# Performance work log

Hardware: AMD Instinct MI355X
Metric: run time of the kernel (lower is better)

The kernel has to match this reference:

```python
import jax, jax.numpy as jnp
import numpy as np

B, IN, H = 16384, 512, 512


def setup_inputs() -> dict:
    key = jax.random.key(0)
    ks = jax.random.split(key, 7)
    s_in = 1.0 / np.sqrt(IN)
    s_h = 1.0 / np.sqrt(H)
    return {
        "x": jax.random.normal(ks[0], (B, IN), jnp.float32),
        "h": jax.random.normal(ks[1], (B, H), jnp.float32),
        "c": jax.random.normal(ks[2], (B, H), jnp.float32),
        # packed gate weights, order [i, f, g, o] along last dim (4*H)
        "Wx": jax.random.normal(ks[3], (IN, 4 * H), jnp.float32) * s_in,
        "Wh": jax.random.normal(ks[4], (H, 4 * H), jnp.float32) * s_h,
        "bx": jax.random.normal(ks[5], (4 * H,), jnp.float32) * s_in,
        "bh": jax.random.normal(ks[6], (4 * H,), jnp.float32) * s_h,
    }


def reference(x, h, c, Wx, Wh, bx, bh):
    # one fused GEMM per input stream instead of 8 small linears; same math
    gates = x @ Wx + bx + h @ Wh + bh          # [B, 4H]
    gi, gf, gg, go = jnp.split(gates, 4, axis=-1)
    i = jax.nn.sigmoid(gi)
    f = jax.nn.sigmoid(gf)
    g = jnp.tanh(gg)
    o = jax.nn.sigmoid(go)
    c_new = f * c + i * g
    h_new = o * jnp.tanh(c_new)
    return (h_new, c_new)
```

## Files before the change

### kernel.cpp

```cpp
#include <hip/hip_runtime.h>
#include <hip/hip_bf16.h>

#define B_DIM   16384
#define IN_DIM  512
#define H_DIM   512
#define K_DIM   1024
#define N4H     2048
#define BH      (B_DIM * H_DIM)

typedef __attribute__((ext_vector_type(8))) short  short8;
typedef __attribute__((ext_vector_type(4))) short  short4v;
typedef __attribute__((ext_vector_type(4))) float  f32x4;

__device__ inline void async_load16(const void* g, void* l) {
    __builtin_amdgcn_global_load_lds(
        (const __attribute__((address_space(1))) void*)g,
        (__attribute__((address_space(3)))       void*)l, 16, 0, 0);
}

__device__ inline short bf16bits(float f) {
    __hip_bfloat16 b = __float2bfloat16(f);
    return *reinterpret_cast<short*>(&b);
}

__device__ inline float sigmoidf_(float v) {
    return 1.0f / (1.0f + __expf(-v));
}
__device__ inline float tanhf_(float v) {
    v = fminf(fmaxf(v, -30.f), 30.f);
    float e = __expf(2.f * v);
    return (e - 1.f) / (e + 1.f);
}

__global__ __launch_bounds__(256) void prep_all(
    const float* __restrict__ Wx, const float* __restrict__ Wh,
    const float* __restrict__ bx, const float* __restrict__ bh,
    const float* __restrict__ x,  const float* __restrict__ h,
    __hip_bfloat16* __restrict__ Wt, __hip_bfloat16* __restrict__ Axh,
    float* __restrict__ bias_p) {
    const int bid = blockIdx.x;
    const int t   = threadIdx.x;

    if (bid < 2048) {
        __shared__ __hip_bfloat16 tile[32][33];
        const int bk = bid & 31;
        const int bn = bid >> 5;
        const int kb = bk * 32, nb = bn * 32;
#pragma unroll
        for (int r = 0; r < 4; ++r) {
            int k_loc = r * 8 + (t >> 5);
            int n_loc = t & 31;
            int kg = kb + k_loc;
            float v = (kg < IN_DIM) ? Wx[(size_t)kg * N4H + nb + n_loc]
                                    : Wh[(size_t)(kg - IN_DIM) * N4H + nb + n_loc];
            tile[k_loc][n_loc] = __float2bfloat16(v);
        }
        __syncthreads();
        {
            int n_loc = t >> 3;
            int k_loc = (t & 7) * 4;
            int ng = nb + n_loc;
            int g  = ng >> 9;
            int c  = ng & 511;
            int row_out = (c >> 5) * 128 + g * 32 + (c & 31);
            short4v v4;
            v4.x = *reinterpret_cast<short*>(&tile[k_loc + 0][n_loc]);
            v4.y = *reinterpret_cast<short*>(&tile[k_loc + 1][n_loc]);
            v4.z = *reinterpret_cast<short*>(&tile[k_loc + 2][n_loc]);
            v4.w = *reinterpret_cast<short*>(&tile[k_loc + 3][n_loc]);
            *(short4v*)&Wt[(size_t)row_out * K_DIM + kb + k_loc] = v4;
        }
        if (bid < 8) {
            int ng = bid * 256 + t;
            int g  = ng >> 9;
            int c  = ng & 511;
            int ro = (c >> 5) * 128 + g * 32 + (c & 31);
            bias_p[ro] = bx[ng] + bh[ng];
        }
    } else {
        const int ab = bid - 2048;
        const int kq = t;
        const float* src = (kq < 128) ? (x + kq * 4)
                                      : (h + (size_t)(kq - 128) * 4);
#pragma unroll
        for (int j = 0; j < 8; ++j) {
            int m = ab * 8 + j;
            float4 v = *(const float4*)(src + (size_t)m * 512);
            short4v sv;
            sv.x = bf16bits(v.x);
            sv.y = bf16bits(v.y);
            sv.z = bf16bits(v.z);
            sv.w = bf16bits(v.w);
            *(short4v*)&Axh[(size_t)m * K_DIM + kq * 4] = sv;
        }
    }
}

__global__ __launch_bounds__(512, 2) void lstm_gemm256(
    const float* __restrict__ c_in,
    const __hip_bfloat16* __restrict__ Axh,
    const __hip_bfloat16* __restrict__ Wt,
    const float* __restrict__ bias_p,
    float* __restrict__ out) {
    __shared__ __align__(16) __hip_bfloat16 lds_a[2][16384];
    __shared__ __align__(16) __hip_bfloat16 lds_b[2][16384];

    const int tid   = threadIdx.x;
    const int w     = tid >> 6;
    const int lane  = tid & 63;
    const int col16 = lane & 15;
    const int quad  = lane >> 4;
    const int wm    = w >> 2;
    const int wn    = w & 3;

    const int jb    = blockIdx.x;
    const int xcd   = jb & 7;
    const int local = jb >> 3;
    const int bm    = xcd * 8 + (local >> 3);
    const int bn    = local & 7;

    f32x4 acc[8][4];
#pragma unroll
    for (int mi = 0; mi < 8; ++mi)
#pragma unroll
        for (int ni = 0; ni < 4; ++ni)
            acc[mi][ni] = (f32x4){0.f, 0.f, 0.f, 0.f};

    const __hip_bfloat16* Ab = Axh + (size_t)bm * 256 * K_DIM;
    const __hip_bfloat16* Bb = Wt  + (size_t)bn * 256 * K_DIM;

    const int lq = ((tid & 3) - ((tid >> 3) & 3)) & 3;

#define STAGE(LDSBUF, GBASE, KH, KT)  do {                                     \
    const __hip_bfloat16* _s = (GBASE) + (size_t)(tid >> 2) * K_DIM            \
                               + (KT) * 64 + (KH) * 32 + lq * 8;               \
    char* _d = (char*)(LDSBUF) + (KH) * 16384 + w * 1024;                      \
    async_load16(_s,                       _d);                                \
    async_load16(_s + (size_t)128 * K_DIM, _d + 8192);                         \
  } while (0)

    int aoff[8], boff[4];
#pragma unroll
    for (int mi = 0; mi < 8; ++mi) {
        int r = wm * 128 + mi * 16 + col16;
        aoff[mi] = r * 64 + ((quad + ((r >> 1) & 3)) & 3) * 16;
    }
#pragma unroll
    for (int ni = 0; ni < 4; ++ni) {
        int r = (wn >> 1) * 128 + ni * 32 + (wn & 1) * 16 + col16;
        boff[ni] = r * 64 + ((quad + ((r >> 1) & 3)) & 3) * 16;
    }

    STAGE(lds_a[0], Ab, 0, 0);
    STAGE(lds_b[0], Bb, 0, 0);
    STAGE(lds_a[0], Ab, 1, 0);
    STAGE(lds_b[0], Bb, 1, 0);

    short8 afrA[4], afrB[4], bfr[4];

#define PHASE_MID()                                                            \
    __builtin_amdgcn_sched_barrier(0);                                         \
    __builtin_amdgcn_s_barrier();                                              \
    asm volatile("s_waitcnt lgkmcnt(0)" ::: "memory");                         \
    __builtin_amdgcn_sched_barrier(0);

    for (int t = 0; t < 16; ++t) {
        const int cur = t & 1;
        const char* la = (const char*)lds_a[cur];
        const char* lb = (const char*)lds_b[cur];
        __hip_bfloat16* nxa = lds_a[cur ^ 1];
        __hip_bfloat16* nxb = lds_b[cur ^ 1];
        const bool pre = (t < 15);

        asm volatile("s_waitcnt vmcnt(4)" ::: "memory");
        __builtin_amdgcn_s_barrier();

#pragma unroll
        for (int q = 0; q < 4; ++q) afrA[q] = *(const short8*)(la + aoff[q]);
#pragma unroll
        for (int n = 0; n < 4; ++n) bfr[n] = *(const short8*)(lb + boff[n]);
        if (pre) STAGE(nxa, Ab, 0, t + 1);
        PHASE_MID();
        __builtin_amdgcn_s_setprio(1);
#pragma unroll
        for (int q = 0; q < 4; ++q)
#pragma unroll
            for (int n = 0; n < 4; ++n)
                acc[q][n] = __builtin_amdgcn_mfma_f32_16x16x32_bf16(
                    afrA[q], bfr[n], acc[q][n], 0, 0, 0);
        __builtin_amdgcn_s_setprio(0);
        __builtin_amdgcn_sched_barrier(0);
        __builtin_amdgcn_s_barrier();

#pragma unroll
        for (int q = 0; q < 4; ++q) afrB[q] = *(const short8*)(la + aoff[q + 4]);
        if (pre) STAGE(nxb, Bb, 0, t + 1);
        PHASE_MID();
        __builtin_amdgcn_s_setprio(1);
#pragma unroll
        for (int q = 0; q < 4; ++q)
#pragma unroll
            for (int n = 0; n < 4; ++n)
                acc[q + 4][n] = __builtin_amdgcn_mfma_f32_16x16x32_bf16(
                    afrB[q], bfr[n], acc[q + 4][n], 0, 0, 0);
        __builtin_amdgcn_s_setprio(0);
        __builtin_amdgcn_sched_barrier(0);
        if (pre) asm volatile("s_waitcnt vmcnt(4)" ::: "memory");
        else     asm volatile("s_waitcnt vmcnt(0)" ::: "memory");
        __builtin_amdgcn_s_barrier();

#pragma unroll
        for (int q = 0; q < 4; ++q) afrA[q] = *(const short8*)(la + 16384 + aoff[q]);
#pragma unroll
        for (int n = 0; n < 4; ++n) bfr[n] = *(const short8*)(lb + 16384 + boff[n]);
        if (pre) STAGE(nxa, Ab, 1, t + 1);
        PHASE_MID();
        __builtin_amdgcn_s_setprio(1);
#pragma unroll
        for (int q = 0; q < 4; ++q)
#pragma unroll
            for (int n = 0; n < 4; ++n)
                acc[q][n] = __builtin_amdgcn_mfma_f32_16x16x32_bf16(
                    afrA[q], bfr[n], acc[q][n], 0, 0, 0);
        __builtin_amdgcn_s_setprio(0);
        __builtin_amdgcn_sched_barrier(0);
        __builtin_amdgcn_s_barrier();

#pragma unroll
        for (int q = 0; q < 4; ++q) afrB[q] = *(const short8*)(la + 16384 + aoff[q + 4]);
        if (pre) STAGE(nxb, Bb, 1, t + 1);
        PHASE_MID();
        __builtin_amdgcn_s_setprio(1);
#pragma unroll
        for (int q = 0; q < 4; ++q)
#pragma unroll
            for (int n = 0; n < 4; ++n)
                acc[q + 4][n] = __builtin_amdgcn_mfma_f32_16x16x32_bf16(
                    afrB[q], bfr[n], acc[q + 4][n], 0, 0, 0);
        __builtin_amdgcn_s_setprio(0);
        __builtin_amdgcn_sched_barrier(0);
        __builtin_amdgcn_s_barrier();
    }
#undef STAGE
#undef PHASE_MID

    float bias_v[4];
#pragma unroll
    for (int g = 0; g < 4; ++g)
        bias_v[g] = bias_p[bn * 256 + (wn >> 1) * 128 + g * 32 + (wn & 1) * 16 + col16];

    const int hc_g = bn * 64 + (wn >> 1) * 32 + (wn & 1) * 16 + col16;

#pragma unroll
    for (int mi = 0; mi < 8; ++mi) {
#pragma unroll
        for (int reg = 0; reg < 4; ++reg) {
            const int m_g = bm * 256 + wm * 128 + mi * 16 + quad * 4 + reg;
            float gi = acc[mi][0][reg] + bias_v[0];
            float gf = acc[mi][1][reg] + bias_v[1];
            float gg = acc[mi][2][reg] + bias_v[2];
            float go = acc[mi][3][reg] + bias_v[3];
            float iv = sigmoidf_(gi);
            float fv = sigmoidf_(gf);
            float gv = tanhf_(gg);
            float ov = sigmoidf_(go);
            float co = c_in[(size_t)m_g * H_DIM + hc_g];
            float cn = fv * co + iv * gv;
            float hn = ov * tanhf_(cn);
            out[(size_t)m_g * H_DIM + hc_g]      = hn;
            out[BH + (size_t)m_g * H_DIM + hc_g] = cn;
        }
    }
}

__global__ __launch_bounds__(256) void prep_weights_fb(
    const float* __restrict__ Wx, const float* __restrict__ Wh,
    const float* __restrict__ bx, const float* __restrict__ bh,
    __hip_bfloat16* __restrict__ Wt, float* __restrict__ bias_p) {
    __shared__ __hip_bfloat16 tile[32][33];
    const int bid = blockIdx.x;
    const int bk  = bid & 31;
    const int bn  = bid >> 5;
    const int t   = threadIdx.x;
    const int kb  = bk * 32, nb = bn * 32;
#pragma unroll
    for (int r = 0; r < 4; ++r) {
        int k_loc = r * 8 + (t >> 5);
        int n_loc = t & 31;
        int kg = kb + k_loc;
        float v = (kg < IN_DIM) ? Wx[(size_t)kg * N4H + nb + n_loc]
                                : Wh[(size_t)(kg - IN_DIM) * N4H + nb + n_loc];
        tile[k_loc][n_loc] = __float2bfloat16(v);
    }
    __syncthreads();
    {
        int n_loc = t >> 3;
        int k_loc = (t & 7) * 4;
        int ng = nb + n_loc;
        int g  = ng >> 9;
        int c  = ng & 511;
        int row_out = (c >> 5) * 128 + g * 32 + (c & 31);
        short4v v4;
        v4.x = *reinterpret_cast<short*>(&tile[k_loc + 0][n_loc]);
        v4.y = *reinterpret_cast<short*>(&tile[k_loc + 1][n_loc]);
        v4.z = *reinterpret_cast<short*>(&tile[k_loc + 2][n_loc]);
        v4.w = *reinterpret_cast<short*>(&tile[k_loc + 3][n_loc]);
        *(short4v*)&Wt[(size_t)row_out * K_DIM + kb + k_loc] = v4;
    }
    if (bid < 8) {
        int ng = bid * 256 + t;
        int g  = ng >> 9;
        int c  = ng & 511;
        int ro = (c >> 5) * 128 + g * 32 + (c & 31);
        bias_p[ro] = bx[ng] + bh[ng];
    }
}

__global__ __launch_bounds__(256, 3) void lstm_gemm_fb(
    const float* __restrict__ x, const float* __restrict__ h,
    const float* __restrict__ c_in,
    const __hip_bfloat16* __restrict__ Wt, const float* __restrict__ bias_p,
    float* __restrict__ out) {
    __shared__ __hip_bfloat16 lds_a[128 * 32];
    __shared__ __hip_bfloat16 lds_b[128 * 32];
    const int tid   = threadIdx.x;
    const int bn    = blockIdx.x & 15;
    const int bm    = blockIdx.x >> 4;
    const int w     = tid >> 6;
    const int lane  = tid & 63;
    const int col16 = lane & 15;
    const int quad  = lane >> 4;
    f32x4 acc[2][8];
#pragma unroll
    for (int mi = 0; mi < 2; ++mi)
#pragma unroll
        for (int ni = 0; ni < 8; ++ni)
            acc[mi][ni] = (f32x4){0.f, 0.f, 0.f, 0.f};
    const __hip_bfloat16* wt_base = Wt + (size_t)(bn * 128) * K_DIM;
    const int chunk0 = w * 2;
    const int e0     = chunk0 * 512 + lane * 8;
    const int bn_loc0 = e0 >> 5, bk_off0 = e0 & 31;
    const int e1     = (chunk0 + 1) * 512 + lane * 8;
    const int bn_loc1 = e1 >> 5, bk_off1 = e1 & 31;
    for (int kt = 0; kt < 32; ++kt) {
        const int kb = kt * 32;
        const float* aptr;
        int koff;
        if (kb < IN_DIM) { aptr = x; koff = kb; }
        else             { aptr = h; koff = kb - IN_DIM; }
        async_load16(wt_base + (size_t)bn_loc0 * K_DIM + kb + bk_off0,
                     (void*)(lds_b + chunk0 * 512));
        async_load16(wt_base + (size_t)bn_loc1 * K_DIM + kb + bk_off1,
                     (void*)(lds_b + (chunk0 + 1) * 512));
        float4 av[4];
#pragma unroll
        for (int j = 0; j < 4; ++j) {
            int cch = j * 256 + tid;
            int row = cch >> 3;
            int kq  = (cch & 7) * 4;
            av[j] = *(const float4*)(aptr + (size_t)(bm * 128 + row) * IN_DIM
                                     + koff + kq);
        }
#pragma unroll
        for (int j = 0; j < 4; ++j) {
            int cch = j * 256 + tid;
            int row = cch >> 3;
            int kq  = (cch & 7) * 4;
            short4v sv;
            sv.x = bf16bits(av[j].x);
            sv.y = bf16bits(av[j].y);
            sv.z = bf16bits(av[j].z);
            sv.w = bf16bits(av[j].w);
            *(short4v*)&lds_a[row * 32 + kq] = sv;
        }
        __syncthreads();
        short8 afr[2], bfr[8];
#pragma unroll
        for (int mi = 0; mi < 2; ++mi)
            afr[mi] = *(const short8*)&lds_a[(w * 32 + mi * 16 + col16) * 32 + quad * 8];
#pragma unroll
        for (int ni = 0; ni < 8; ++ni)
            bfr[ni] = *(const short8*)&lds_b[(ni * 16 + col16) * 32 + quad * 8];
#pragma unroll
        for (int mi = 0; mi < 2; ++mi)
#pragma unroll
            for (int ni = 0; ni < 8; ++ni)
                acc[mi][ni] = __builtin_amdgcn_mfma_f32_16x16x32_bf16(
                    afr[mi], bfr[ni], acc[mi][ni], 0, 0, 0);
        __syncthreads();
    }
    float bias_v[4][2];
#pragma unroll
    for (int g = 0; g < 4; ++g)
#pragma unroll
        for (int h2 = 0; h2 < 2; ++h2)
            bias_v[g][h2] = bias_p[bn * 128 + g * 32 + h2 * 16 + col16];
#pragma unroll
    for (int mi = 0; mi < 2; ++mi) {
#pragma unroll
        for (int reg = 0; reg < 4; ++reg) {
            const int m_g = bm * 128 + w * 32 + mi * 16 + quad * 4 + reg;
#pragma unroll
            for (int h2 = 0; h2 < 2; ++h2) {
                const int hc_g = bn * 32 + h2 * 16 + col16;
                float gi = acc[mi][0 + h2][reg] + bias_v[0][h2];
                float gf = acc[mi][2 + h2][reg] + bias_v[1][h2];
                float gg = acc[mi][4 + h2][reg] + bias_v[2][h2];
                float go = acc[mi][6 + h2][reg] + bias_v[3][h2];
                float iv = sigmoidf_(gi);
                float fv = sigmoidf_(gf);
                float gv = tanhf_(gg);
                float ov = sigmoidf_(go);
                float co = c_in[(size_t)m_g * H_DIM + hc_g];
                float cn = fv * co + iv * gv;
                float hn = ov * tanhf_(cn);
                out[(size_t)m_g * H_DIM + hc_g]      = hn;
                out[BH + (size_t)m_g * H_DIM + hc_g] = cn;
            }
        }
    }
}

extern "C" void kernel_launch(void* const* d_in, const int* in_sizes, int n_in,
                              void* d_out, int out_size, void* d_ws, size_t ws_size,
                              hipStream_t stream) {
    const float* x  = (const float*)d_in[0];
    const float* h  = (const float*)d_in[1];
    const float* c  = (const float*)d_in[2];
    const float* Wx = (const float*)d_in[3];
    const float* Wh = (const float*)d_in[4];
    const float* bx = (const float*)d_in[5];
    const float* bh = (const float*)d_in[6];

    const size_t wtBytes  = (size_t)N4H * K_DIM * 2;
    const size_t axhBytes = (size_t)B_DIM * K_DIM * 2;
    const size_t need     = wtBytes + axhBytes + (size_t)N4H * 4;

    if (ws_size >= need) {
        __hip_bfloat16* Wt  = (__hip_bfloat16*)d_ws;
        __hip_bfloat16* Axh = (__hip_bfloat16*)((char*)d_ws + wtBytes);
        float* bias_p = (float*)((char*)d_ws + wtBytes + axhBytes);
        prep_all<<<4096, 256, 0, stream>>>(Wx, Wh, bx, bh, x, h, Wt, Axh, bias_p);
        lstm_gemm256<<<512, 512, 0, stream>>>(c, Axh, Wt, bias_p, (float*)d_out);
    } else {
        __hip_bfloat16* Wt = (__hip_bfloat16*)d_ws;
        float* bias_p = (float*)((char*)d_ws + wtBytes);
        prep_weights_fb<<<2048, 256, 0, stream>>>(Wx, Wh, bx, bh, Wt, bias_p);
        lstm_gemm_fb<<<2048, 256, 0, stream>>>(x, h, c, Wt, bias_p, (float*)d_out);
    }
}
```

Measured before the change: 243.0 us.

## Merge GEMM K-loop phases, drop XCD block swizzle, widen prep grid

Each K half-tile is now processed in one phase: all eight A fragments load into registers, both A and B prefetches issue together, and 32 MFMAs run per barrier, where before the work was split into two phases of 16 MFMAs. This halves the barrier count per iteration at the cost of more VGPRs for fragments. The XCD-aware block-index remapping is replaced with a plain row-major mapping, which may change L2 reuse across XCDs. The activation-conversion part of the prep kernel now does 4 rows per block over more blocks (6144 total) to raise parallelism.

```diff
diff --git a/kernel.cpp b/kernel.cpp
--- a/kernel.cpp
+++ b/kernel.cpp
@@ -83,8 +83,8 @@
         const float* src = (kq < 128) ? (x + kq * 4)
                                       : (h + (size_t)(kq - 128) * 4);
 #pragma unroll
-        for (int j = 0; j < 8; ++j) {
-            int m = ab * 8 + j;
+        for (int j = 0; j < 4; ++j) {
+            int m = ab * 4 + j;
             float4 v = *(const float4*)(src + (size_t)m * 512);
             short4v sv;
             sv.x = bf16bits(v.x);
@@ -113,11 +113,9 @@
     const int wm    = w >> 2;
     const int wn    = w & 3;
 
-    const int jb    = blockIdx.x;
-    const int xcd   = jb & 7;
-    const int local = jb >> 3;
-    const int bm    = xcd * 8 + (local >> 3);
-    const int bn    = local & 7;
+    const int jb = blockIdx.x;
+    const int bn = jb & 7;
+    const int bm = jb >> 3;
 
     f32x4 acc[8][4];
 #pragma unroll
@@ -156,14 +154,6 @@
     STAGE(lds_a[0], Ab, 1, 0);
     STAGE(lds_b[0], Bb, 1, 0);
 
-    short8 afrA[4], afrB[4], bfr[4];
-
-#define PHASE_MID()                                                            \
-    __builtin_amdgcn_sched_barrier(0);                                         \
-    __builtin_amdgcn_s_barrier();                                              \
-    asm volatile("s_waitcnt lgkmcnt(0)" ::: "memory");                         \
-    __builtin_amdgcn_sched_barrier(0);
-
     for (int t = 0; t < 16; ++t) {
         const int cur = t & 1;
         const char* la = (const char*)lds_a[cur];
@@ -175,34 +165,24 @@
         asm volatile("s_waitcnt vmcnt(4)" ::: "memory");
         __builtin_amdgcn_s_barrier();
 
-#pragma unroll
-        for (int q = 0; q < 4; ++q) afrA[q] = *(const short8*)(la + aoff[q]);
+        short8 afr[8], bfr[4];
+
+#pragma unroll
+        for (int q = 0; q < 8; ++q) afr[q] = *(const short8*)(la + aoff[q]);
 #pragma unroll
         for (int n = 0; n < 4; ++n) bfr[n] = *(const short8*)(lb + boff[n]);
-        if (pre) STAGE(nxa, Ab, 0, t + 1);
-        PHASE_MID();
+        if (pre) { STAGE(nxa, Ab, 0, t + 1); STAGE(nxb, Bb, 0, t + 1); }
+        __builtin_amdgcn_sched_barrier(0);
+        __builtin_amdgcn_s_barrier();
+        asm volatile("s_waitcnt lgkmcnt(0)" ::: "memory");
+        __builtin_amdgcn_sched_barrier(0);
         __builtin_amdgcn_s_setprio(1);
 #pragma unroll
-        for (int q = 0; q < 4; ++q)
+        for (int q = 0; q < 8; ++q)
 #pragma unroll
             for (int n = 0; n < 4; ++n)
                 acc[q][n] = __builtin_amdgcn_mfma_f32_16x16x32_bf16(
-                    afrA[q], bfr[n], acc[q][n], 0, 0, 0);
-        __builtin_amdgcn_s_setprio(0);
-        __builtin_amdgcn_sched_barrier(0);
-        __builtin_amdgcn_s_barrier();
-
-#pragma unroll
-        for (int q = 0; q < 4; ++q) afrB[q] = *(const short8*)(la + aoff[q + 4]);
-        if (pre) STAGE(nxb, Bb, 0, t + 1);
-        PHASE_MID();
-        __builtin_amdgcn_s_setprio(1);
-#pragma unroll
-        for (int q = 0; q < 4; ++q)
-#pragma unroll
-            for (int n = 0; n < 4; ++n)
-                acc[q + 4][n] = __builtin_amdgcn_mfma_f32_16x16x32_bf16(
-                    afrB[q], bfr[n], acc[q + 4][n], 0, 0, 0);
+                    afr[q], bfr[n], acc[q][n], 0, 0, 0);
         __builtin_amdgcn_s_setprio(0);
         __builtin_amdgcn_sched_barrier(0);
         if (pre) asm volatile("s_waitcnt vmcnt(4)" ::: "memory");
@@ -210,39 +190,26 @@
         __builtin_amdgcn_s_barrier();
 
 #pragma unroll
-        for (int q = 0; q < 4; ++q) afrA[q] = *(const short8*)(la + 16384 + aoff[q]);
+        for (int q = 0; q < 8; ++q) afr[q] = *(const short8*)(la + 16384 + aoff[q]);
 #pragma unroll
         for (int n = 0; n < 4; ++n) bfr[n] = *(const short8*)(lb + 16384 + boff[n]);
-        if (pre) STAGE(nxa, Ab, 1, t + 1);
-        PHASE_MID();
+        if (pre) { STAGE(nxa, Ab, 1, t + 1); STAGE(nxb, Bb, 1, t + 1); }
+        __builtin_amdgcn_sched_barrier(0);
+        __builtin_amdgcn_s_barrier();
+        asm volatile("s_waitcnt lgkmcnt(0)" ::: "memory");
+        __builtin_amdgcn_sched_barrier(0);
         __builtin_amdgcn_s_setprio(1);
 #pragma unroll
-        for (int q = 0; q < 4; ++q)
+        for (int q = 0; q < 8; ++q)
 #pragma unroll
             for (int n = 0; n < 4; ++n)
                 acc[q][n] = __builtin_amdgcn_mfma_f32_16x16x32_bf16(
-                    afrA[q], bfr[n], acc[q][n], 0, 0, 0);
+                    afr[q], bfr[n], acc[q][n], 0, 0, 0);
         __builtin_amdgcn_s_setprio(0);
         __builtin_amdgcn_sched_barrier(0);
         __builtin_amdgcn_s_barrier();
-
-#pragma unroll
-        for (int q = 0; q < 4; ++q) afrB[q] = *(const short8*)(la + 16384 + aoff[q + 4]);
-        if (pre) STAGE(nxb, Bb, 1, t + 1);
-        PHASE_MID();
-        __builtin_amdgcn_s_setprio(1);
-#pragma unroll
-        for (int q = 0; q < 4; ++q)
-#pragma unroll
-            for (int n = 0; n < 4; ++n)
-                acc[q + 4][n] = __builtin_amdgcn_mfma_f32_16x16x32_bf16(
-                    afrB[q], bfr[n], acc[q + 4][n], 0, 0, 0);
-        __builtin_amdgcn_s_setprio(0);
-        __builtin_amdgcn_sched_barrier(0);
-        __builtin_amdgcn_s_barrier();
     }
 #undef STAGE
-#undef PHASE_MID
 
     float bias_v[4];
 #pragma unroll
@@ -440,7 +407,7 @@
         __hip_bfloat16* Wt  = (__hip_bfloat16*)d_ws;
         __hip_bfloat16* Axh = (__hip_bfloat16*)((char*)d_ws + wtBytes);
         float* bias_p = (float*)((char*)d_ws + wtBytes + axhBytes);
-        prep_all<<<4096, 256, 0, stream>>>(Wx, Wh, bx, bh, x, h, Wt, Axh, bias_p);
+        prep_all<<<6144, 256, 0, stream>>>(Wx, Wh, bx, bh, x, h, Wt, Axh, bias_p);
         lstm_gemm256<<<512, 512, 0, stream>>>(c, Axh, Wt, bias_p, (float*)d_out);
     } else {
         __hip_bfloat16* Wt = (__hip_bfloat16*)d_ws;
```

After: 235.9 us. -2.9%, faster.
